# Kernel optimization log

Measured on AMD Instinct MI355X. Metric: run time of the kernel, lower is better.

## Reference

```python
import jax, jax.numpy as jnp
import numpy as np

EMBED, ACT, DETER, STOCH, HID = 1536, 10, 2048, 64, 1024
T, B = 64, 256
LN_EPS = 1e-3


def _ln(x, s, b):
    mu = jnp.mean(x, axis=-1, keepdims=True)
    var = jnp.mean(jnp.square(x - mu), axis=-1, keepdims=True)
    return (x - mu) * jax.lax.rsqrt(var + LN_EPS) * s + b


def setup_inputs() -> dict:
    key = jax.random.key(0)
    ks = jax.random.split(key, 20)
    g = lambda k, shp, fan: jax.random.normal(k, shp, jnp.float32) * (1.0 / np.sqrt(fan))
    inp = {
        "embeds": jax.random.normal(ks[0], (T, B, EMBED), jnp.float32),
        "actions": jax.random.normal(ks[1], (T, B, ACT), jnp.float32),
        "h_t": jnp.zeros((B, DETER), jnp.float32),
        "z_t": jnp.zeros((B, STOCH), jnp.float32),
        "noise": jax.random.normal(ks[2], (T, B, STOCH), jnp.float32),
        # DeterNext
        "z_mlp_w": g(ks[3], (HID // 2, STOCH), STOCH),
        "z_mlp_b": jnp.zeros((HID // 2,), jnp.float32),
        "a_mlp_w": g(ks[4], (HID // 2, ACT), ACT),  # bias=False
        "ln_za_s": jnp.ones((HID,), jnp.float32),
        "ln_za_b": jnp.zeros((HID,), jnp.float32),
        # GRUCell (torch layout: [3*deter, in])
        "gru_wih": g(ks[5], (3 * DETER, HID), HID),
        "gru_whh": g(ks[6], (3 * DETER, DETER), DETER),
        "gru_bih": jnp.zeros((3 * DETER,), jnp.float32),
        "gru_bhh": jnp.zeros((3 * DETER,), jnp.float32),
        # PosteriorNext
        "post_h_w": g(ks[7], (HID, DETER), DETER),
        "post_h_b": jnp.zeros((HID,), jnp.float32),
        "post_e_w": g(ks[8], (HID, EMBED), EMBED),
        "post_e_b": jnp.zeros((HID,), jnp.float32),
        "ln_post_s": jnp.ones((HID,), jnp.float32),
        "ln_post_b": jnp.zeros((HID,), jnp.float32),
        "post_w": g(ks[9], (2 * STOCH, HID), HID),
        "post_b": jnp.zeros((2 * STOCH,), jnp.float32),
        # PriorNext
        "prior_h_w": g(ks[10], (HID, DETER), DETER),
        "prior_h_b": jnp.zeros((HID,), jnp.float32),
        "ln_prior_s": jnp.ones((HID,), jnp.float32),
        "ln_prior_b": jnp.zeros((HID,), jnp.float32),
        "prior_w": g(ks[11], (2 * STOCH, HID), HID),
        "prior_b": jnp.zeros((2 * STOCH,), jnp.float32),
    }
    return inp


def _rssm_forward(embeds, actions, h0, z0, noise,
                  z_mlp_w, z_mlp_b, a_mlp_w, ln_za_s, ln_za_b,
                  gru_wih, gru_whh, gru_bih, gru_bhh,
                  post_h_w, post_h_b, post_e_w, post_e_b, ln_post_s, ln_post_b,
                  post_w, post_b,
                  prior_h_w, prior_h_b, ln_prior_s, ln_prior_b, prior_w, prior_b):
    def step(carry, xs):
        h, z = carry
        e, a, n = xs
        # DeterNext: concat(z_mlp(z), a_mlp(a)) -> LN -> ELU
        x = jnp.concatenate([z @ z_mlp_w.T + z_mlp_b, a @ a_mlp_w.T], axis=-1)
        za = jax.nn.elu(_ln(x, ln_za_s, ln_za_b))
        # GRUCell
        gi = za @ gru_wih.T + gru_bih
        gh = h @ gru_whh.T + gru_bhh
        ir, iu, ic = jnp.split(gi, 3, axis=-1)
        hr, hu, hc = jnp.split(gh, 3, axis=-1)
        r = jax.nn.sigmoid(ir + hr)
        u = jax.nn.sigmoid(iu + hu)
        c = jnp.tanh(ic + r * hc)
        h1 = (1.0 - u) * c + u * h
        # PosteriorNext
        p = jax.nn.elu(_ln(h1 @ post_h_w.T + post_h_b + e @ post_e_w.T + post_e_b,
                           ln_post_s, ln_post_b))
        post = p @ post_w.T + post_b  # [B, 2*stoch]
        mean, sraw = jnp.split(post, 2, axis=-1)
        std = 2.0 * jax.nn.sigmoid(sraw) + 0.1
        z1 = mean + std * n  # rsample with externally-supplied noise
        return (h1, z1), (post, h1, z1)

    (_, _), (posts, states_h, post_z_samples) = jax.lax.scan(
        step, (h0, z0), (embeds, actions, noise))
    # batch prior over all timesteps
    pr = jax.nn.elu(_ln(states_h @ prior_h_w.T + prior_h_b, ln_prior_s, ln_prior_b))
    priors = pr @ prior_w.T + prior_b  # [T, B, 2*stoch]
    features = jnp.concatenate([states_h, post_z_samples], axis=-1)  # [T,B,deter+stoch]
    return priors, posts, post_z_samples, features


def reference(embeds, actions, h_t, z_t, noise,
              z_mlp_w, z_mlp_b, a_mlp_w, ln_za_s, ln_za_b,
              gru_wih, gru_whh, gru_bih, gru_bhh,
              post_h_w, post_h_b, post_e_w, post_e_b, ln_post_s, ln_post_b,
              post_w, post_b,
              prior_h_w, prior_h_b, ln_prior_s, ln_prior_b, prior_w, prior_b):
    return _rssm_forward(embeds, actions, h_t, z_t, noise,
                         z_mlp_w, z_mlp_b, a_mlp_w, ln_za_s, ln_za_b,
                         gru_wih, gru_whh, gru_bih, gru_bhh,
                         post_h_w, post_h_b, post_e_w, post_e_b, ln_post_s, ln_post_b,
                         post_w, post_b,
                         prior_h_w, prior_h_b, ln_prior_s, ln_prior_b, prior_w, prior_b)
```

## Files before the change

kernel.cpp:

```cpp
#include <hip/hip_runtime.h>

#define LN_EPS 1e-3f

typedef short s8v __attribute__((ext_vector_type(8)));
typedef short s4v __attribute__((ext_vector_type(4)));
typedef float f4v __attribute__((ext_vector_type(4)));
typedef unsigned short u16;

__device__ __forceinline__ u16 f2bf(float f) {
  unsigned int x = __float_as_uint(f);
  x += 0x7fffu + ((x >> 16) & 1u);
  return (u16)(x >> 16);
}
__device__ __forceinline__ float bf2f(u16 u) {
  return __uint_as_float(((unsigned int)u) << 16);
}

__global__ void k_cvt(const float* __restrict__ src, u16* __restrict__ dst, int n) {
  int i = blockIdx.x * blockDim.x + threadIdx.x;
  int stride = gridDim.x * blockDim.x;
  for (; i < n; i += stride) dst[i] = f2bf(src[i]);
}

__global__ void k_pack(const float* __restrict__ wih, const float* __restrict__ whh,
                       u16* __restrict__ wp) {
  size_t i4 = ((size_t)blockIdx.x * 256 + threadIdx.x) * 4;
  int n = (int)(i4 / 3072);
  int k = (int)(i4 % 3072);
  int g = n >> 11;
  int j = n & 2047;
  s4v v;
#pragma unroll
  for (int q = 0; q < 4; ++q) {
    int kk = k + q;
    float x = 0.f;
    if (g <= 1) {
      x = (kk < 1024) ? wih[(size_t)(g * 2048 + j) * 1024 + kk]
                      : whh[(size_t)(g * 2048 + j) * 2048 + kk - 1024];
    } else if (g == 2) {
      x = (kk < 1024) ? wih[(size_t)(4096 + j) * 1024 + kk] : 0.f;
    } else {
      x = (kk >= 1024) ? whh[(size_t)(4096 + j) * 2048 + kk - 1024] : 0.f;
    }
    v[q] = (short)f2bf(x);
  }
  *(s4v*)(wp + i4) = v;
}

__global__ void k_hinit(const float* __restrict__ h0, float* __restrict__ hf,
                        u16* __restrict__ acat) {
  int i = blockIdx.x * 256 + threadIdx.x;
  int b = i >> 11, j = i & 2047;
  float v = h0[i];
  hf[i] = v;
  acat[(size_t)b * 3072 + 1024 + j] = f2bf(v);
}

template <bool AF32, bool OUTBF16, bool GRUKR>
__global__ __launch_bounds__(512) void k_gemm8(
    const void* __restrict__ Av, int lda, const u16* __restrict__ Bw, int ldb,
    int ks0, int ke0, float* __restrict__ Cf, u16* __restrict__ Cb, int ldc,
    const float* __restrict__ bias, const u16* __restrict__ extra) {
  int bx, by, ks = ks0, ke = ke0;
  if (GRUKR) {
    int hw = blockIdx.x;
    int logical = (hw & 7) * 32 + (hw >> 3);
    bx = logical & 3;
    by = logical >> 2;
    if (by < 32) { ks = 0; ke = 48; }
    else if (by < 48) { ks = 0; ke = 16; }
    else { ks = 16; ke = 48; }
  } else {
    bx = blockIdx.x;
    by = blockIdx.y;
  }
  const int tid = threadIdx.x;
  const int m0 = bx * 64;
  const int n0 = by * 128;
  __shared__ __align__(16) u16 As[64][72];
  __shared__ __align__(16) u16 Bs[128][72];
  const int lane = tid & 63;
  const int w = tid >> 6;
  const int wr = w >> 2;
  const int wc = w & 3;
  const int lr = lane & 15;
  const int lk = lane >> 4;

  f4v acc[2][2];
#pragma unroll
  for (int m = 0; m < 2; ++m)
#pragma unroll
    for (int n = 0; n < 2; ++n) acc[m][n] = (f4v)(0.0f);

  for (int s = ks; s < ke; ++s) {
    const int k0 = s << 6;
    {
      int row = tid >> 3, k8 = (tid & 7) << 3;
      if (AF32) {
        const float* ap = (const float*)Av + (size_t)(m0 + row) * lda + k0 + k8;
        float4 f0 = *(const float4*)ap;
        float4 f1 = *(const float4*)(ap + 4);
        s8v v;
        v[0] = (short)f2bf(f0.x); v[1] = (short)f2bf(f0.y);
        v[2] = (short)f2bf(f0.z); v[3] = (short)f2bf(f0.w);
        v[4] = (short)f2bf(f1.x); v[5] = (short)f2bf(f1.y);
        v[6] = (short)f2bf(f1.z); v[7] = (short)f2bf(f1.w);
        *(s8v*)&As[row][k8] = v;
      } else {
        *(s8v*)&As[row][k8] =
            *(const s8v*)((const u16*)Av + (size_t)(m0 + row) * lda + k0 + k8);
      }
    }
#pragma unroll
    for (int it = 0; it < 2; ++it) {
      int c = tid + it * 512;
      int row = c >> 3, k8 = (c & 7) << 3;
      *(s8v*)&Bs[row][k8] = *(const s8v*)(Bw + (size_t)(n0 + row) * ldb + k0 + k8);
    }
    __syncthreads();
#pragma unroll
    for (int kk = 0; kk < 2; ++kk) {
      const int koff = kk * 32 + lk * 8;
      s8v a[2], b[2];
      a[0] = *(const s8v*)&As[wr * 32 + lr][koff];
      a[1] = *(const s8v*)&As[wr * 32 + 16 + lr][koff];
      b[0] = *(const s8v*)&Bs[wc * 32 + lr][koff];
      b[1] = *(const s8v*)&Bs[wc * 32 + 16 + lr][koff];
#pragma unroll
      for (int m = 0; m < 2; ++m)
#pragma unroll
        for (int n = 0; n < 2; ++n)
          acc[m][n] =
              __builtin_amdgcn_mfma_f32_16x16x32_bf16(a[m], b[n], acc[m][n], 0, 0, 0);
    }
    __syncthreads();
  }
#pragma unroll
  for (int m = 0; m < 2; ++m) {
#pragma unroll
    for (int n = 0; n < 2; ++n) {
#pragma unroll
      for (int r = 0; r < 4; ++r) {
        int row = m0 + wr * 32 + m * 16 + lk * 4 + r;
        int col = n0 + wc * 32 + n * 16 + lr;
        float v = acc[m][n][r];
        if (bias) v += bias[col];
        if (extra) v += bf2f(extra[(size_t)row * ldc + col]);
        if (OUTBF16)
          Cb[(size_t)row * ldc + col] = f2bf(v);
        else
          Cf[(size_t)row * ldc + col] = v;
      }
    }
  }
}

__global__ __launch_bounds__(256) void k_za(
    const float* __restrict__ zsrc, const float* __restrict__ act,
    const float* __restrict__ zw, const float* __restrict__ zb,
    const float* __restrict__ aw, const float* __restrict__ lns,
    const float* __restrict__ lnb, u16* __restrict__ acat) {
  const int b = blockIdx.x, tid = threadIdx.x;
  __shared__ float zsh[64];
  __shared__ float ash[16];
  __shared__ float red[256];
  if (tid < 64) zsh[tid] = zsrc[b * 64 + tid];
  if (tid < 10) ash[tid] = act[b * 10 + tid];
  __syncthreads();
  float x[4];
#pragma unroll
  for (int i = 0; i < 2; ++i) {
    int c = tid + i * 256;
    const float* wp = zw + c * 64;
    float a = zb[c];
#pragma unroll
    for (int k = 0; k < 64; ++k) a += zsh[k] * wp[k];
    x[i] = a;
  }
#pragma unroll
  for (int i = 2; i < 4; ++i) {
    int c2 = tid + (i - 2) * 256;
    const float* wp = aw + c2 * 10;
    float a = 0.f;
#pragma unroll
    for (int k = 0; k < 10; ++k) a += ash[k] * wp[k];
    x[i] = a;
  }
  float s = x[0] + x[1] + x[2] + x[3];
  red[tid] = s;
  __syncthreads();
  for (int o = 128; o > 0; o >>= 1) {
    if (tid < o) red[tid] += red[tid + o];
    __syncthreads();
  }
  float mu = red[0] * (1.0f / 1024.0f);
  __syncthreads();
  float q = 0.f;
#pragma unroll
  for (int i = 0; i < 4; ++i) {
    float d = x[i] - mu;
    q += d * d;
  }
  red[tid] = q;
  __syncthreads();
  for (int o = 128; o > 0; o >>= 1) {
    if (tid < o) red[tid] += red[tid + o];
    __syncthreads();
  }
  float rs = rsqrtf(red[0] * (1.0f / 1024.0f) + LN_EPS);
#pragma unroll
  for (int i = 0; i < 4; ++i) {
    int c = tid + i * 256;
    float y = (x[i] - mu) * rs * lns[c] + lnb[c];
    y = y > 0.f ? y : expm1f(y);
    acat[(size_t)b * 3072 + c] = f2bf(y);
  }
}

__global__ __launch_bounds__(256) void k_gate(
    const float* __restrict__ gout, const float* __restrict__ bih,
    const float* __restrict__ bhh, float* __restrict__ hf,
    u16* __restrict__ acat, float* __restrict__ feat, int t) {
  int idx = blockIdx.x * 256 + threadIdx.x;
  int b = idx >> 11, j = idx & 2047;
  size_t rb = (size_t)b * 8192;
  float vr = gout[rb + j] + bih[j] + bhh[j];
  float vu = gout[rb + 2048 + j] + bih[2048 + j] + bhh[2048 + j];
  float ic = gout[rb + 4096 + j] + bih[4096 + j];
  float hc = gout[rb + 6144 + j] + bhh[4096 + j];
  float r = 1.f / (1.f + expf(-vr));
  float u = 1.f / (1.f + expf(-vu));
  float c = tanhf(ic + r * hc);
  float h1 = (1.f - u) * c + u * hf[idx];
  hf[idx] = h1;
  acat[(size_t)b * 3072 + 1024 + j] = f2bf(h1);
  feat[(size_t)(t * 256 + b) * 2112 + j] = h1;
}

template <bool SRCBF16>
__global__ __launch_bounds__(256) void k_lnelu(const void* __restrict__ xsrc,
                                               const float* __restrict__ s,
                                               const float* __restrict__ bb,
                                               u16* __restrict__ out) {
  int row = blockIdx.x, tid = threadIdx.x;
  __shared__ float red[256];
  float v[4];
#pragma unroll
  for (int i = 0; i < 4; ++i) {
    size_t idx = (size_t)row * 1024 + tid + i * 256;
    v[i] = SRCBF16 ? bf2f(((const u16*)xsrc)[idx]) : ((const float*)xsrc)[idx];
  }
  float sm = v[0] + v[1] + v[2] + v[3];
  red[tid] = sm;
  __syncthreads();
  for (int o = 128; o > 0; o >>= 1) {
    if (tid < o) red[tid] += red[tid + o];
    __syncthreads();
  }
  float mu = red[0] * (1.0f / 1024.0f);
  __syncthreads();
  float q = 0.f;
#pragma unroll
  for (int i = 0; i < 4; ++i) {
    float d = v[i] - mu;
    q += d * d;
  }
  red[tid] = q;
  __syncthreads();
  for (int o = 128; o > 0; o >>= 1) {
    if (tid < o) red[tid] += red[tid + o];
    __syncthreads();
  }
  float rs = rsqrtf(red[0] * (1.0f / 1024.0f) + LN_EPS);
#pragma unroll
  for (int i = 0; i < 4; ++i) {
    int c = tid + i * 256;
    float y = (v[i] - mu) * rs * s[c] + bb[c];
    y = y > 0.f ? y : expm1f(y);
    out[(size_t)row * 1024 + c] = f2bf(y);
  }
}

__global__ __launch_bounds__(512) void k_postz(
    const u16* __restrict__ Ab, const u16* __restrict__ Bw,
    const float* __restrict__ bias, float* __restrict__ posts_t,
    const float* __restrict__ noise_t, float* __restrict__ zout,
    float* __restrict__ feat, int t) {
  const int tid = threadIdx.x;
  const int m0 = blockIdx.x * 64;
  __shared__ __align__(16) u16 As[64][72];
  __shared__ __align__(16) u16 Bs[128][72];
  __shared__ float ps[64][132];
  const int lane = tid & 63;
  const int w = tid >> 6;
  const int wr = w >> 2;
  const int wc = w & 3;
  const int lr = lane & 15;
  const int lk = lane >> 4;

  f4v acc[2][2];
#pragma unroll
  for (int m = 0; m < 2; ++m)
#pragma unroll
    for (int n = 0; n < 2; ++n) acc[m][n] = (f4v)(0.0f);

  for (int s = 0; s < 16; ++s) {
    const int k0 = s << 6;
    {
      int row = tid >> 3, k8 = (tid & 7) << 3;
      *(s8v*)&As[row][k8] =
          *(const s8v*)(Ab + (size_t)(m0 + row) * 1024 + k0 + k8);
    }
#pragma unroll
    for (int it = 0; it < 2; ++it) {
      int c = tid + it * 512;
      int row = c >> 3, k8 = (c & 7) << 3;
      *(s8v*)&Bs[row][k8] = *(const s8v*)(Bw + (size_t)row * 1024 + k0 + k8);
    }
    __syncthreads();
#pragma unroll
    for (int kk = 0; kk < 2; ++kk) {
      const int koff = kk * 32 + lk * 8;
      s8v a[2], b[2];
      a[0] = *(const s8v*)&As[wr * 32 + lr][koff];
      a[1] = *(const s8v*)&As[wr * 32 + 16 + lr][koff];
      b[0] = *(const s8v*)&Bs[wc * 32 + lr][koff];
      b[1] = *(const s8v*)&Bs[wc * 32 + 16 + lr][koff];
#pragma unroll
      for (int m = 0; m < 2; ++m)
#pragma unroll
        for (int n = 0; n < 2; ++n)
          acc[m][n] =
              __builtin_amdgcn_mfma_f32_16x16x32_bf16(a[m], b[n], acc[m][n], 0, 0, 0);
    }
    __syncthreads();
  }
#pragma unroll
  for (int m = 0; m < 2; ++m) {
#pragma unroll
    for (int n = 0; n < 2; ++n) {
#pragma unroll
      for (int r = 0; r < 4; ++r) {
        int lrow = wr * 32 + m * 16 + lk * 4 + r;
        int col = wc * 32 + n * 16 + lr;
        float v = acc[m][n][r] + bias[col];
        posts_t[(size_t)(m0 + lrow) * 128 + col] = v;
        ps[lrow][col] = v;
      }
    }
  }
  __syncthreads();
#pragma unroll
  for (int q = 0; q < 8; ++q) {
    int e = tid * 8 + q;
    int row = e >> 6, j = e & 63;
    float mean = ps[row][j];
    float sraw = ps[row][64 + j];
    float sd = 2.f / (1.f + expf(-sraw)) + 0.1f;
    float z = mean + sd * noise_t[(m0 + row) * 64 + j];
    zout[(m0 + row) * 64 + j] = z;
    feat[(size_t)(t * 256 + m0 + row) * 2112 + 2048 + j] = z;
  }
}

extern "C" void kernel_launch(void* const* d_in, const int* in_sizes, int n_in,
                              void* d_out, int out_size, void* d_ws,
                              size_t ws_size, hipStream_t stream) {
  const float* embeds = (const float*)d_in[0];
  const float* actions = (const float*)d_in[1];
  const float* h_t = (const float*)d_in[2];
  const float* z_t = (const float*)d_in[3];
  const float* noise = (const float*)d_in[4];
  const float* z_mlp_w = (const float*)d_in[5];
  const float* z_mlp_b = (const float*)d_in[6];
  const float* a_mlp_w = (const float*)d_in[7];
  const float* ln_za_s = (const float*)d_in[8];
  const float* ln_za_b = (const float*)d_in[9];
  const float* gru_wih = (const float*)d_in[10];
  const float* gru_whh = (const float*)d_in[11];
  const float* gru_bih = (const float*)d_in[12];
  const float* gru_bhh = (const float*)d_in[13];
  const float* post_h_w = (const float*)d_in[14];
  const float* post_h_b = (const float*)d_in[15];
  const float* post_e_w = (const float*)d_in[16];
  const float* post_e_b = (const float*)d_in[17];
  const float* ln_post_s = (const float*)d_in[18];
  const float* ln_post_b = (const float*)d_in[19];
  const float* post_w = (const float*)d_in[20];
  const float* post_b = (const float*)d_in[21];
  const float* prior_h_w = (const float*)d_in[22];
  const float* prior_h_b = (const float*)d_in[23];
  const float* ln_prior_s = (const float*)d_in[24];
  const float* ln_prior_b = (const float*)d_in[25];
  const float* prior_w = (const float*)d_in[26];
  const float* prior_b = (const float*)d_in[27];

  float* out = (float*)d_out;
  float* out_priors = out;
  float* out_posts = out + 2097152;
  float* out_z = out + 4194304;
  float* out_feat = out + 5242880;

  char* ws = (char*)d_ws;
  size_t off = 0;
  auto alloc = [&](size_t bytes) {
    char* p = ws + off;
    off += (bytes + 255) & ~(size_t)255;
    return p;
  };
  char* regW = alloc((size_t)8192 * 3072 * 2);
  u16* wpack = (u16*)regW;
  u16* prx_b = (u16*)regW;
  u16* posth_b = (u16*)alloc((size_t)1024 * 2048 * 2);
  u16* priorh_b = (u16*)alloc((size_t)1024 * 2048 * 2);
  u16* postw_b = (u16*)alloc((size_t)128 * 1024 * 2);
  u16* priorw_b = (u16*)alloc((size_t)128 * 1024 * 2);
  u16* poste_b = (u16*)alloc((size_t)1024 * 1536 * 2);
  u16* acat = (u16*)alloc((size_t)256 * 3072 * 2);
  float* hf = (float*)alloc((size_t)256 * 2048 * 4);
  float* xbuf = (float*)alloc((size_t)256 * 1024 * 4);
  u16* p_b = (u16*)alloc((size_t)256 * 1024 * 2);
  char* regU = alloc((size_t)42 * 1024 * 1024);
  u16* e_part = (u16*)regU;
  float* gout = (float*)(regU + 33554432);
  u16* p_pr = (u16*)regU;

  k_pack<<<24576, 256, 0, stream>>>(gru_wih, gru_whh, wpack);
  k_cvt<<<512, 256, 0, stream>>>(post_h_w, posth_b, 1024 * 2048);
  k_cvt<<<512, 256, 0, stream>>>(prior_h_w, priorh_b, 1024 * 2048);
  k_cvt<<<64, 256, 0, stream>>>(post_w, postw_b, 128 * 1024);
  k_cvt<<<64, 256, 0, stream>>>(prior_w, priorw_b, 128 * 1024);
  k_cvt<<<512, 256, 0, stream>>>(post_e_w, poste_b, 1024 * 1536);
  k_hinit<<<2048, 256, 0, stream>>>(h_t, hf, acat);

  k_gemm8<true, true, false><<<dim3(256, 8), 512, 0, stream>>>(
      embeds, 1536, poste_b, 1536, 0, 24, nullptr, e_part, 1024, post_e_b,
      nullptr);

  for (int t = 0; t < 64; ++t) {
    const float* zsrc = (t == 0) ? z_t : (out_z + (size_t)(t - 1) * 16384);
    k_za<<<256, 256, 0, stream>>>(zsrc, actions + (size_t)t * 2560, z_mlp_w,
                                  z_mlp_b, a_mlp_w, ln_za_s, ln_za_b, acat);
    k_gemm8<false, false, true><<<256, 512, 0, stream>>>(
        acat, 3072, wpack, 3072, 0, 48, gout, nullptr, 8192, nullptr, nullptr);
    k_gate<<<2048, 256, 0, stream>>>(gout, gru_bih, gru_bhh, hf, acat,
                                     out_feat, t);
    k_gemm8<false, false, false><<<dim3(4, 8), 512, 0, stream>>>(
        acat + 1024, 3072, posth_b, 2048, 0, 32, xbuf, nullptr, 1024, post_h_b,
        e_part + (size_t)t * 262144);
    k_lnelu<false><<<256, 256, 0, stream>>>(xbuf, ln_post_s, ln_post_b, p_b);
    k_postz<<<4, 512, 0, stream>>>(p_b, postw_b, post_b,
                                   out_posts + (size_t)t * 32768,
                                   noise + (size_t)t * 16384,
                                   out_z + (size_t)t * 16384, out_feat, t);
  }

  k_gemm8<true, true, false><<<dim3(256, 8), 512, 0, stream>>>(
      out_feat, 2112, priorh_b, 2048, 0, 32, nullptr, prx_b, 1024, prior_h_b,
      nullptr);
  k_lnelu<true><<<16384, 256, 0, stream>>>(prx_b, ln_prior_s, ln_prior_b, p_pr);
  k_gemm8<false, false, false><<<dim3(256, 1), 512, 0, stream>>>(
      p_pr, 1024, priorw_b, 1024, 0, 16, out_priors, nullptr, 128, prior_b,
      nullptr);
}
```

Before: 8.537 ms.

## Fuse GRU gates into pre-packed GEMM, add async LDS loads, fuse posterior LN

```diff
diff --git a/kernel.cpp b/kernel.cpp
--- a/kernel.cpp
+++ b/kernel.cpp
@@ -3,7 +3,6 @@
 #define LN_EPS 1e-3f
 
 typedef short s8v __attribute__((ext_vector_type(8)));
-typedef short s4v __attribute__((ext_vector_type(4)));
 typedef float f4v __attribute__((ext_vector_type(4)));
 typedef unsigned short u16;
 
@@ -16,35 +15,69 @@
   return __uint_as_float(((unsigned int)u) << 16);
 }
 
+__device__ __forceinline__ void glds16(const u16* g, void* l) {
+  __builtin_amdgcn_global_load_lds(
+      (const __attribute__((address_space(1))) void*)g,
+      (__attribute__((address_space(3))) void*)l, 16, 0, 0);
+}
+
 __global__ void k_cvt(const float* __restrict__ src, u16* __restrict__ dst, int n) {
   int i = blockIdx.x * blockDim.x + threadIdx.x;
   int stride = gridDim.x * blockDim.x;
   for (; i < n; i += stride) dst[i] = f2bf(src[i]);
 }
 
-__global__ void k_pack(const float* __restrict__ wih, const float* __restrict__ whh,
-                       u16* __restrict__ wp) {
-  size_t i4 = ((size_t)blockIdx.x * 256 + threadIdx.x) * 4;
-  int n = (int)(i4 / 3072);
-  int k = (int)(i4 % 3072);
-  int g = n >> 11;
-  int j = n & 2047;
-  s4v v;
-#pragma unroll
-  for (int q = 0; q < 4; ++q) {
-    int kk = k + q;
-    float x = 0.f;
-    if (g <= 1) {
-      x = (kk < 1024) ? wih[(size_t)(g * 2048 + j) * 1024 + kk]
-                      : whh[(size_t)(g * 2048 + j) * 2048 + kk - 1024];
-    } else if (g == 2) {
-      x = (kk < 1024) ? wih[(size_t)(4096 + j) * 1024 + kk] : 0.f;
+__global__ void k_packgru(const float* __restrict__ wih,
+                          const float* __restrict__ whh, u16* __restrict__ wt) {
+  int u = blockIdx.x * 256 + threadIdx.x;
+  int nt = u / 73728;
+  int r1 = u % 73728;
+  int s = r1 / 1536;
+  int r2 = r1 % 1536;
+  int sub = r2 / 512;
+  int r3 = r2 % 512;
+  int ch = r3 / 64;
+  int row = r3 % 64;
+  int j = nt * 64 + row;
+  int kbase = s * 64 + ch * 8;
+  s8v v;
+#pragma unroll
+  for (int e = 0; e < 8; ++e) {
+    int kk = kbase + e;
+    float x;
+    if (sub == 0) {
+      x = kk < 1024 ? wih[(size_t)j * 1024 + kk] : whh[(size_t)j * 2048 + kk - 1024];
+    } else if (sub == 1) {
+      int jj = 2048 + j;
+      x = kk < 1024 ? wih[(size_t)jj * 1024 + kk] : whh[(size_t)jj * 2048 + kk - 1024];
     } else {
-      x = (kk >= 1024) ? whh[(size_t)(4096 + j) * 2048 + kk - 1024] : 0.f;
-    }
-    v[q] = (short)f2bf(x);
-  }
-  *(s4v*)(wp + i4) = v;
+      int jj = 4096 + j;
+      x = (s < 16) ? wih[(size_t)jj * 1024 + kk] : whh[(size_t)jj * 2048 + kk - 1024];
+    }
+    v[e] = (short)f2bf(x);
+  }
+  *(s8v*)(wt + (size_t)u * 8) = v;
+}
+
+__global__ void k_packB(const float* __restrict__ src, u16* __restrict__ dst,
+                        int K, int BN, int total) {
+  int u = blockIdx.x * 256 + threadIdx.x;
+  if (u >= total) return;
+  int ns = K >> 6;
+  int perNt = ns * 8 * BN;
+  int nt = u / perNt;
+  int r1 = u % perNt;
+  int s = r1 / (8 * BN);
+  int r2 = r1 % (8 * BN);
+  int ch = r2 / BN;
+  int row = r2 % BN;
+  int j = nt * BN + row;
+  int k = s * 64 + ch * 8;
+  const float* sp = src + (size_t)j * K + k;
+  s8v v;
+#pragma unroll
+  for (int e = 0; e < 8; ++e) v[e] = (short)f2bf(sp[e]);
+  *(s8v*)(dst + (size_t)u * 8) = v;
 }
 
 __global__ void k_hinit(const float* __restrict__ h0, float* __restrict__ hf,
@@ -56,24 +89,348 @@
   acat[(size_t)b * 3072 + 1024 + j] = f2bf(v);
 }
 
-template <bool AF32, bool OUTBF16, bool GRUKR>
+__global__ __launch_bounds__(256) void k_za(
+    const float* __restrict__ zsrc, const float* __restrict__ act,
+    const float* __restrict__ zw, const float* __restrict__ zb,
+    const float* __restrict__ aw, const float* __restrict__ lns,
+    const float* __restrict__ lnb, u16* __restrict__ acat) {
+  const int b = blockIdx.x, tid = threadIdx.x;
+  __shared__ float zsh[64];
+  __shared__ float ash[12];
+  __shared__ float wred[8];
+  if (tid < 64) zsh[tid] = zsrc[b * 64 + tid];
+  if (tid < 10) ash[tid] = act[b * 10 + tid];
+  __syncthreads();
+  float x[4];
+#pragma unroll
+  for (int i = 0; i < 2; ++i) {
+    int c = tid + i * 256;
+    const float4* wp = (const float4*)(zw + c * 64);
+    float a = zb[c];
+#pragma unroll
+    for (int k = 0; k < 16; ++k) {
+      float4 v = wp[k];
+      a += zsh[k * 4] * v.x + zsh[k * 4 + 1] * v.y + zsh[k * 4 + 2] * v.z +
+           zsh[k * 4 + 3] * v.w;
+    }
+    x[i] = a;
+  }
+#pragma unroll
+  for (int i = 2; i < 4; ++i) {
+    int c2 = tid + (i - 2) * 256;
+    const float* wp = aw + c2 * 10;
+    float a = 0.f;
+#pragma unroll
+    for (int k = 0; k < 10; ++k) a += ash[k] * wp[k];
+    x[i] = a;
+  }
+  float s = x[0] + x[1] + x[2] + x[3];
+#pragma unroll
+  for (int o = 1; o < 64; o <<= 1) s += __shfl_xor(s, o);
+  if ((tid & 63) == 0) wred[tid >> 6] = s;
+  __syncthreads();
+  float mu = (wred[0] + wred[1] + wred[2] + wred[3]) * (1.f / 1024.f);
+  float q = 0.f;
+#pragma unroll
+  for (int i = 0; i < 4; ++i) {
+    float d = x[i] - mu;
+    q += d * d;
+  }
+#pragma unroll
+  for (int o = 1; o < 64; o <<= 1) q += __shfl_xor(q, o);
+  if ((tid & 63) == 0) wred[4 + (tid >> 6)] = q;
+  __syncthreads();
+  float rs = rsqrtf((wred[4] + wred[5] + wred[6] + wred[7]) * (1.f / 1024.f) + LN_EPS);
+  int cols[4] = {tid, tid + 256, 512 + tid, 768 + tid};
+#pragma unroll
+  for (int i = 0; i < 4; ++i) {
+    int c = cols[i];
+    float y = (x[i] - mu) * rs * lns[c] + lnb[c];
+    y = y > 0.f ? y : expm1f(y);
+    acat[(size_t)b * 3072 + c] = f2bf(y);
+  }
+}
+
+__global__ __launch_bounds__(256) void k_gru(
+    const u16* __restrict__ acat_r, const u16* __restrict__ wt,
+    const float* __restrict__ bih, const float* __restrict__ bhh,
+    const float* __restrict__ hf_r, float* __restrict__ hf_w,
+    u16* __restrict__ acat_w, float* __restrict__ feat, int t) {
+  const int hw = blockIdx.x;
+  const int logical = (hw & 7) * 32 + (hw >> 3);
+  const int mg = logical & 7;
+  const int nt = logical >> 3;
+  const int m0 = mg * 32;
+  const int tid = threadIdx.x;
+  const int lane = tid & 63;
+  const int w = tid >> 6;
+  const int lr = lane & 15, lk = lane >> 4;
+
+  __shared__ __align__(16) char smem[2][28672];
+
+  const int arow = 8 * w + (lane >> 3);
+  const int acol8 = ((lane & 7) ^ (arow & 7)) * 8;
+  const u16* aSrc = acat_r + (size_t)(m0 + arow) * 3072 + acol8;
+  const u16* wtNt = wt + (size_t)nt * 48 * 3 * 4096;
+
+  f4v accr[2], accu[2], acci[2], acch[2];
+  accr[0] = accr[1] = accu[0] = accu[1] = (f4v)(0.f);
+  acci[0] = acci[1] = acch[0] = acch[1] = (f4v)(0.f);
+
+#define K1_STAGE(BB, S) { \
+    char* base = &smem[BB][0]; \
+    glds16(aSrc + (S) * 64, base + w * 1024); \
+    const u16* bsrc = wtNt + (size_t)(S) * 3 * 4096; \
+    _Pragma("unroll") for (int i = 0; i < 6; ++i) { \
+      int cf = w + i * 4; \
+      glds16(bsrc + (cf * 64 + lane) * 8, base + 4096 + cf * 1024); \
+    } }
+
+#define K1_COMP(BB, ACCX) { \
+    char* base = &smem[BB][0]; \
+    _Pragma("unroll") for (int kk = 0; kk < 2; ++kk) { \
+      int ch = kk * 4 + lk; \
+      int r0 = lr, r1 = 16 + lr; \
+      s8v a0 = *(const s8v*)(base + r0 * 128 + ((ch ^ (r0 & 7)) * 16)); \
+      s8v a1 = *(const s8v*)(base + r1 * 128 + ((ch ^ (r1 & 7)) * 16)); \
+      int rb = (w * 16 + lr) * 16; \
+      s8v br = *(const s8v*)(base + 4096 + ch * 1024 + rb); \
+      s8v bu = *(const s8v*)(base + 12288 + ch * 1024 + rb); \
+      s8v bx = *(const s8v*)(base + 20480 + ch * 1024 + rb); \
+      accr[0] = __builtin_amdgcn_mfma_f32_16x16x32_bf16(a0, br, accr[0], 0, 0, 0); \
+      accr[1] = __builtin_amdgcn_mfma_f32_16x16x32_bf16(a1, br, accr[1], 0, 0, 0); \
+      accu[0] = __builtin_amdgcn_mfma_f32_16x16x32_bf16(a0, bu, accu[0], 0, 0, 0); \
+      accu[1] = __builtin_amdgcn_mfma_f32_16x16x32_bf16(a1, bu, accu[1], 0, 0, 0); \
+      ACCX[0] = __builtin_amdgcn_mfma_f32_16x16x32_bf16(a0, bx, ACCX[0], 0, 0, 0); \
+      ACCX[1] = __builtin_amdgcn_mfma_f32_16x16x32_bf16(a1, bx, ACCX[1], 0, 0, 0); \
+    } }
+
+  K1_STAGE(0, 0)
+  int buf = 0;
+  for (int s = 0; s < 16; ++s) {
+    asm volatile("s_waitcnt vmcnt(0)" ::: "memory");
+    __builtin_amdgcn_s_barrier();
+    __builtin_amdgcn_sched_barrier(0);
+    K1_STAGE(buf ^ 1, s + 1)
+    K1_COMP(buf, acci)
+    buf ^= 1;
+  }
+  for (int s = 16; s < 48; ++s) {
+    asm volatile("s_waitcnt vmcnt(0)" ::: "memory");
+    __builtin_amdgcn_s_barrier();
+    __builtin_amdgcn_sched_barrier(0);
+    if (s + 1 < 48) K1_STAGE(buf ^ 1, s + 1)
+    K1_COMP(buf, acch)
+    buf ^= 1;
+  }
+
+  const int j = nt * 64 + w * 16 + lr;
+  const float b_ri = bih[j], b_rh = bhh[j];
+  const float b_ui = bih[2048 + j], b_uh = bhh[2048 + j];
+  const float b_ci = bih[4096 + j], b_ch = bhh[4096 + j];
+#pragma unroll
+  for (int m = 0; m < 2; ++m) {
+#pragma unroll
+    for (int r = 0; r < 4; ++r) {
+      int grow = m0 + m * 16 + lk * 4 + r;
+      float vr = accr[m][r] + b_ri + b_rh;
+      float vu = accu[m][r] + b_ui + b_uh;
+      float ic = acci[m][r] + b_ci;
+      float hc = acch[m][r] + b_ch;
+      float rg = 1.f / (1.f + expf(-vr));
+      float ug = 1.f / (1.f + expf(-vu));
+      float c = tanhf(ic + rg * hc);
+      float hold = hf_r[(size_t)grow * 2048 + j];
+      float h1 = (1.f - ug) * c + ug * hold;
+      hf_w[(size_t)grow * 2048 + j] = h1;
+      acat_w[(size_t)grow * 3072 + 1024 + j] = f2bf(h1);
+      feat[(size_t)(t * 256 + grow) * 2112 + j] = h1;
+    }
+  }
+#undef K1_STAGE
+#undef K1_COMP
+}
+
+__global__ __launch_bounds__(256) void k_post(
+    const u16* __restrict__ acat_h, const u16* __restrict__ wp,
+    const float* __restrict__ bias, const u16* __restrict__ epart_t,
+    float* __restrict__ xbuf) {
+  const int bx = blockIdx.x;
+  const int mg = bx & 7, nt = bx >> 3;
+  const int m0 = mg * 32;
+  const int tid = threadIdx.x;
+  const int lane = tid & 63;
+  const int w = tid >> 6;
+  const int lr = lane & 15, lk = lane >> 4;
+
+  __shared__ __align__(16) char smem[2][12288];
+
+  const int arow = 8 * w + (lane >> 3);
+  const int acol8 = ((lane & 7) ^ (arow & 7)) * 8;
+  const u16* aSrc = acat_h + (size_t)(m0 + arow) * 3072 + 1024 + acol8;
+  const u16* wpNt = wp + (size_t)nt * 32 * 4096;
+
+  f4v acc[2];
+  acc[0] = (f4v)(0.f);
+  acc[1] = (f4v)(0.f);
+
+#define K2_STAGE(BB, S) { \
+    char* base = &smem[BB][0]; \
+    glds16(aSrc + (S) * 64, base + w * 1024); \
+    const u16* bsrc = wpNt + (size_t)(S) * 4096; \
+    _Pragma("unroll") for (int i = 0; i < 2; ++i) { \
+      int cf = w + i * 4; \
+      glds16(bsrc + (cf * 64 + lane) * 8, base + 4096 + cf * 1024); \
+    } }
+
+  K2_STAGE(0, 0)
+  int buf = 0;
+  for (int s = 0; s < 32; ++s) {
+    asm volatile("s_waitcnt vmcnt(0)" ::: "memory");
+    __builtin_amdgcn_s_barrier();
+    __builtin_amdgcn_sched_barrier(0);
+    if (s + 1 < 32) K2_STAGE(buf ^ 1, s + 1)
+    char* base = &smem[buf][0];
+#pragma unroll
+    for (int kk = 0; kk < 2; ++kk) {
+      int ch = kk * 4 + lk;
+      int r0 = lr, r1 = 16 + lr;
+      s8v a0 = *(const s8v*)(base + r0 * 128 + ((ch ^ (r0 & 7)) * 16));
+      s8v a1 = *(const s8v*)(base + r1 * 128 + ((ch ^ (r1 & 7)) * 16));
+      s8v b = *(const s8v*)(base + 4096 + ch * 1024 + (w * 16 + lr) * 16);
+      acc[0] = __builtin_amdgcn_mfma_f32_16x16x32_bf16(a0, b, acc[0], 0, 0, 0);
+      acc[1] = __builtin_amdgcn_mfma_f32_16x16x32_bf16(a1, b, acc[1], 0, 0, 0);
+    }
+    buf ^= 1;
+  }
+  const int col = nt * 64 + w * 16 + lr;
+#pragma unroll
+  for (int m = 0; m < 2; ++m) {
+#pragma unroll
+    for (int r = 0; r < 4; ++r) {
+      int grow = m0 + m * 16 + lk * 4 + r;
+      float v = acc[m][r] + bias[col] + bf2f(epart_t[(size_t)grow * 1024 + col]);
+      xbuf[(size_t)grow * 1024 + col] = v;
+    }
+  }
+#undef K2_STAGE
+}
+
+__global__ __launch_bounds__(512) void k_postz(
+    const float* __restrict__ xb, const u16* __restrict__ pw,
+    const float* __restrict__ lns, const float* __restrict__ lnb,
+    const float* __restrict__ pb, float* __restrict__ posts_t,
+    const float* __restrict__ noise_t, float* __restrict__ zout,
+    float* __restrict__ feat, int t) {
+  const int m0 = blockIdx.x * 32;
+  const int tid = threadIdx.x;
+  const int lane = tid & 63;
+  const int w = tid >> 6;
+  const int lr = lane & 15, lk = lane >> 4;
+  __shared__ __align__(16) u16 As[2][32][64];
+  __shared__ __align__(16) u16 Bs[2][8][128][8];
+  __shared__ float lmu[32], lrs[32];
+  __shared__ float ps[32][132];
+  {
+    int row = tid >> 4, sg = tid & 15;
+    const float4* xp = (const float4*)(xb + (size_t)(m0 + row) * 1024 + sg * 64);
+    float s = 0.f, q = 0.f;
+#pragma unroll
+    for (int i = 0; i < 16; ++i) {
+      float4 v = xp[i];
+      s += v.x + v.y + v.z + v.w;
+      q += v.x * v.x + v.y * v.y + v.z * v.z + v.w * v.w;
+    }
+#pragma unroll
+    for (int o = 1; o < 16; o <<= 1) {
+      s += __shfl_xor(s, o);
+      q += __shfl_xor(q, o);
+    }
+    if (sg == 0) {
+      float mu = s * (1.f / 1024.f);
+      lmu[row] = mu;
+      lrs[row] = rsqrtf(q * (1.f / 1024.f) - mu * mu + LN_EPS);
+    }
+  }
+  __syncthreads();
+
+#define K3_STAGEA(BB, S) if (tid < 256) { \
+    int row = tid >> 3, k8 = tid & 7; \
+    const float* xp = xb + (size_t)(m0 + row) * 1024 + (S) * 64 + k8 * 8; \
+    float mu = lmu[row], rs = lrs[row]; \
+    s8v v; \
+    _Pragma("unroll") for (int e = 0; e < 8; ++e) { \
+      int c = (S) * 64 + k8 * 8 + e; \
+      float y = (xp[e] - mu) * rs * lns[c] + lnb[c]; \
+      y = y > 0.f ? y : expm1f(y); \
+      v[e] = (short)f2bf(y); \
+    } \
+    *(s8v*)((char*)&As[BB][0][0] + row * 128 + ((k8 ^ (row & 7)) * 16)) = v; }
+
+#define K3_STAGEB(BB, S) { \
+    const u16* bsrc = pw + (size_t)(S) * 8192; \
+    glds16(bsrc + (((w >> 1) * 128 + (w & 1) * 64 + lane) * 8), \
+           (char*)&Bs[BB][0][0][0] + w * 1024); \
+    glds16(bsrc + ((((w >> 1) + 4) * 128 + (w & 1) * 64 + lane) * 8), \
+           (char*)&Bs[BB][0][0][0] + w * 1024 + 8192); }
+
+  f4v acc[2];
+  acc[0] = (f4v)(0.f);
+  acc[1] = (f4v)(0.f);
+  K3_STAGEA(0, 0)
+  K3_STAGEB(0, 0)
+  __syncthreads();
+  int buf = 0;
+  for (int s = 0; s < 16; ++s) {
+    if (s + 1 < 16) {
+      K3_STAGEA(buf ^ 1, s + 1)
+      K3_STAGEB(buf ^ 1, s + 1)
+    }
+#pragma unroll
+    for (int kk = 0; kk < 2; ++kk) {
+      int ch = kk * 4 + lk;
+      int r0 = lr, r1 = 16 + lr;
+      s8v a0 = *(const s8v*)((char*)&As[buf][0][0] + r0 * 128 + ((ch ^ (r0 & 7)) * 16));
+      s8v a1 = *(const s8v*)((char*)&As[buf][0][0] + r1 * 128 + ((ch ^ (r1 & 7)) * 16));
+      s8v b = *(const s8v*)((char*)&Bs[buf][0][0][0] + ch * 2048 + (w * 16 + lr) * 16);
+      acc[0] = __builtin_amdgcn_mfma_f32_16x16x32_bf16(a0, b, acc[0], 0, 0, 0);
+      acc[1] = __builtin_amdgcn_mfma_f32_16x16x32_bf16(a1, b, acc[1], 0, 0, 0);
+    }
+    __syncthreads();
+    buf ^= 1;
+  }
+#pragma unroll
+  for (int m = 0; m < 2; ++m) {
+#pragma unroll
+    for (int r = 0; r < 4; ++r) {
+      int row = m * 16 + lk * 4 + r;
+      int col = w * 16 + lr;
+      float v = acc[m][r] + pb[col];
+      posts_t[(size_t)(m0 + row) * 128 + col] = v;
+      ps[row][col] = v;
+    }
+  }
+  __syncthreads();
+#pragma unroll
+  for (int q = 0; q < 4; ++q) {
+    int e = q * 512 + tid;
+    int row = e >> 6, j = e & 63;
+    float mean = ps[row][j], sraw = ps[row][64 + j];
+    float sd = 2.f / (1.f + expf(-sraw)) + 0.1f;
+    float z = mean + sd * noise_t[(m0 + row) * 64 + j];
+    zout[(m0 + row) * 64 + j] = z;
+    feat[(size_t)(t * 256 + m0 + row) * 2112 + 2048 + j] = z;
+  }
+#undef K3_STAGEA
+#undef K3_STAGEB
+}
+
+template <bool AF32, bool OUTBF16>
 __global__ __launch_bounds__(512) void k_gemm8(
     const void* __restrict__ Av, int lda, const u16* __restrict__ Bw, int ldb,
-    int ks0, int ke0, float* __restrict__ Cf, u16* __restrict__ Cb, int ldc,
-    const float* __restrict__ bias, const u16* __restrict__ extra) {
-  int bx, by, ks = ks0, ke = ke0;
-  if (GRUKR) {
-    int hw = blockIdx.x;
-    int logical = (hw & 7) * 32 + (hw >> 3);
-    bx = logical & 3;
-    by = logical >> 2;
-    if (by < 32) { ks = 0; ke = 48; }
-    else if (by < 48) { ks = 0; ke = 16; }
-    else { ks = 16; ke = 48; }
-  } else {
-    bx = blockIdx.x;
-    by = blockIdx.y;
-  }
+    int nstage, float* __restrict__ Cf, u16* __restrict__ Cb, int ldc,
+    const float* __restrict__ bias) {
+  const int bx = blockIdx.x, by = blockIdx.y;
   const int tid = threadIdx.x;
   const int m0 = bx * 64;
   const int n0 = by * 128;
@@ -92,7 +449,7 @@
 #pragma unroll
     for (int n = 0; n < 2; ++n) acc[m][n] = (f4v)(0.0f);
 
-  for (int s = ks; s < ke; ++s) {
+  for (int s = 0; s < nstage; ++s) {
     const int k0 = s << 6;
     {
       int row = tid >> 3, k8 = (tid & 7) << 3;
@@ -145,7 +502,6 @@
         int col = n0 + wc * 32 + n * 16 + lr;
         float v = acc[m][n][r];
         if (bias) v += bias[col];
-        if (extra) v += bf2f(extra[(size_t)row * ldc + col]);
         if (OUTBF16)
           Cb[(size_t)row * ldc + col] = f2bf(v);
         else
@@ -155,90 +511,7 @@
   }
 }
 
-__global__ __launch_bounds__(256) void k_za(
-    const float* __restrict__ zsrc, const float* __restrict__ act,
-    const float* __restrict__ zw, const float* __restrict__ zb,
-    const float* __restrict__ aw, const float* __restrict__ lns,
-    const float* __restrict__ lnb, u16* __restrict__ acat) {
-  const int b = blockIdx.x, tid = threadIdx.x;
-  __shared__ float zsh[64];
-  __shared__ float ash[16];
-  __shared__ float red[256];
-  if (tid < 64) zsh[tid] = zsrc[b * 64 + tid];
-  if (tid < 10) ash[tid] = act[b * 10 + tid];
-  __syncthreads();
-  float x[4];
-#pragma unroll
-  for (int i = 0; i < 2; ++i) {
-    int c = tid + i * 256;
-    const float* wp = zw + c * 64;
-    float a = zb[c];
-#pragma unroll
-    for (int k = 0; k < 64; ++k) a += zsh[k] * wp[k];
-    x[i] = a;
-  }
-#pragma unroll
-  for (int i = 2; i < 4; ++i) {
-    int c2 = tid + (i - 2) * 256;
-    const float* wp = aw + c2 * 10;
-    float a = 0.f;
-#pragma unroll
-    for (int k = 0; k < 10; ++k) a += ash[k] * wp[k];
-    x[i] = a;
-  }
-  float s = x[0] + x[1] + x[2] + x[3];
-  red[tid] = s;
-  __syncthreads();
-  for (int o = 128; o > 0; o >>= 1) {
-    if (tid < o) red[tid] += red[tid + o];
-    __syncthreads();
-  }
-  float mu = red[0] * (1.0f / 1024.0f);
-  __syncthreads();
-  float q = 0.f;
-#pragma unroll
-  for (int i = 0; i < 4; ++i) {
-    float d = x[i] - mu;
-    q += d * d;
-  }
-  red[tid] = q;
-  __syncthreads();
-  for (int o = 128; o > 0; o >>= 1) {
-    if (tid < o) red[tid] += red[tid + o];
-    __syncthreads();
-  }
-  float rs = rsqrtf(red[0] * (1.0f / 1024.0f) + LN_EPS);
-#pragma unroll
-  for (int i = 0; i < 4; ++i) {
-    int c = tid + i * 256;
-    float y = (x[i] - mu) * rs * lns[c] + lnb[c];
-    y = y > 0.f ? y : expm1f(y);
-    acat[(size_t)b * 3072 + c] = f2bf(y);
-  }
-}
-
-__global__ __launch_bounds__(256) void k_gate(
-    const float* __restrict__ gout, const float* __restrict__ bih,
-    const float* __restrict__ bhh, float* __restrict__ hf,
-    u16* __restrict__ acat, float* __restrict__ feat, int t) {
-  int idx = blockIdx.x * 256 + threadIdx.x;
-  int b = idx >> 11, j = idx & 2047;
-  size_t rb = (size_t)b * 8192;
-  float vr = gout[rb + j] + bih[j] + bhh[j];
-  float vu = gout[rb + 2048 + j] + bih[2048 + j] + bhh[2048 + j];
-  float ic = gout[rb + 4096 + j] + bih[4096 + j];
-  float hc = gout[rb + 6144 + j] + bhh[4096 + j];
-  float r = 1.f / (1.f + expf(-vr));
-  float u = 1.f / (1.f + expf(-vu));
-  float c = tanhf(ic + r * hc);
-  float h1 = (1.f - u) * c + u * hf[idx];
-  hf[idx] = h1;
-  acat[(size_t)b * 3072 + 1024 + j] = f2bf(h1);
-  feat[(size_t)(t * 256 + b) * 2112 + j] = h1;
-}
-
-template <bool SRCBF16>
-__global__ __launch_bounds__(256) void k_lnelu(const void* __restrict__ xsrc,
+__global__ __launch_bounds__(256) void k_lnelu(const u16* __restrict__ xsrc,
                                                const float* __restrict__ s,
                                                const float* __restrict__ bb,
                                                u16* __restrict__ out) {
@@ -248,7 +521,7 @@
 #pragma unroll
   for (int i = 0; i < 4; ++i) {
     size_t idx = (size_t)row * 1024 + tid + i * 256;
-    v[i] = SRCBF16 ? bf2f(((const u16*)xsrc)[idx]) : ((const float*)xsrc)[idx];
+    v[i] = bf2f(xsrc[idx]);
   }
   float sm = v[0] + v[1] + v[2] + v[3];
   red[tid] = sm;
@@ -278,88 +551,6 @@
     float y = (v[i] - mu) * rs * s[c] + bb[c];
     y = y > 0.f ? y : expm1f(y);
     out[(size_t)row * 1024 + c] = f2bf(y);
-  }
-}
-
-__global__ __launch_bounds__(512) void k_postz(
-    const u16* __restrict__ Ab, const u16* __restrict__ Bw,
-    const float* __restrict__ bias, float* __restrict__ posts_t,
-    const float* __restrict__ noise_t, float* __restrict__ zout,
-    float* __restrict__ feat, int t) {
-  const int tid = threadIdx.x;
-  const int m0 = blockIdx.x * 64;
-  __shared__ __align__(16) u16 As[64][72];
-  __shared__ __align__(16) u16 Bs[128][72];
-  __shared__ float ps[64][132];
-  const int lane = tid & 63;
-  const int w = tid >> 6;
-  const int wr = w >> 2;
-  const int wc = w & 3;
-  const int lr = lane & 15;
-  const int lk = lane >> 4;
-
-  f4v acc[2][2];
-#pragma unroll
-  for (int m = 0; m < 2; ++m)
-#pragma unroll
-    for (int n = 0; n < 2; ++n) acc[m][n] = (f4v)(0.0f);
-
-  for (int s = 0; s < 16; ++s) {
-    const int k0 = s << 6;
-    {
-      int row = tid >> 3, k8 = (tid & 7) << 3;
-      *(s8v*)&As[row][k8] =
-          *(const s8v*)(Ab + (size_t)(m0 + row) * 1024 + k0 + k8);
-    }
-#pragma unroll
-    for (int it = 0; it < 2; ++it) {
-      int c = tid + it * 512;
-      int row = c >> 3, k8 = (c & 7) << 3;
-      *(s8v*)&Bs[row][k8] = *(const s8v*)(Bw + (size_t)row * 1024 + k0 + k8);
-    }
-    __syncthreads();
-#pragma unroll
-    for (int kk = 0; kk < 2; ++kk) {
-      const int koff = kk * 32 + lk * 8;
-      s8v a[2], b[2];
-      a[0] = *(const s8v*)&As[wr * 32 + lr][koff];
-      a[1] = *(const s8v*)&As[wr * 32 + 16 + lr][koff];
-      b[0] = *(const s8v*)&Bs[wc * 32 + lr][koff];
-      b[1] = *(const s8v*)&Bs[wc * 32 + 16 + lr][koff];
-#pragma unroll
-      for (int m = 0; m < 2; ++m)
-#pragma unroll
-        for (int n = 0; n < 2; ++n)
-          acc[m][n] =
-              __builtin_amdgcn_mfma_f32_16x16x32_bf16(a[m], b[n], acc[m][n], 0, 0, 0);
-    }
-    __syncthreads();
-  }
-#pragma unroll
-  for (int m = 0; m < 2; ++m) {
-#pragma unroll
-    for (int n = 0; n < 2; ++n) {
-#pragma unroll
-      for (int r = 0; r < 4; ++r) {
-        int lrow = wr * 32 + m * 16 + lk * 4 + r;
-        int col = wc * 32 + n * 16 + lr;
-        float v = acc[m][n][r] + bias[col];
-        posts_t[(size_t)(m0 + lrow) * 128 + col] = v;
-        ps[lrow][col] = v;
-      }
-    }
-  }
-  __syncthreads();
-#pragma unroll
-  for (int q = 0; q < 8; ++q) {
-    int e = tid * 8 + q;
-    int row = e >> 6, j = e & 63;
-    float mean = ps[row][j];
-    float sraw = ps[row][64 + j];
-    float sd = 2.f / (1.f + expf(-sraw)) + 0.1f;
-    float z = mean + sd * noise_t[(m0 + row) * 64 + j];
-    zout[(m0 + row) * 64 + j] = z;
-    feat[(size_t)(t * 256 + m0 + row) * 2112 + 2048 + j] = z;
   }
 }
 
@@ -408,58 +599,55 @@
     off += (bytes + 255) & ~(size_t)255;
     return p;
   };
-  char* regW = alloc((size_t)8192 * 3072 * 2);
-  u16* wpack = (u16*)regW;
+  char* regW = alloc((size_t)32 * 48 * 3 * 4096 * 2);
+  u16* wt = (u16*)regW;
   u16* prx_b = (u16*)regW;
-  u16* posth_b = (u16*)alloc((size_t)1024 * 2048 * 2);
+  u16* posthP = (u16*)alloc((size_t)1024 * 2048 * 2);
+  u16* postwP = (u16*)alloc((size_t)128 * 1024 * 2);
+  u16* poste_b = (u16*)alloc((size_t)1024 * 1536 * 2);
   u16* priorh_b = (u16*)alloc((size_t)1024 * 2048 * 2);
-  u16* postw_b = (u16*)alloc((size_t)128 * 1024 * 2);
   u16* priorw_b = (u16*)alloc((size_t)128 * 1024 * 2);
-  u16* poste_b = (u16*)alloc((size_t)1024 * 1536 * 2);
-  u16* acat = (u16*)alloc((size_t)256 * 3072 * 2);
-  float* hf = (float*)alloc((size_t)256 * 2048 * 4);
+  u16* acat0 = (u16*)alloc((size_t)256 * 3072 * 2);
+  u16* acat1 = (u16*)alloc((size_t)256 * 3072 * 2);
+  float* hf0 = (float*)alloc((size_t)256 * 2048 * 4);
+  float* hf1 = (float*)alloc((size_t)256 * 2048 * 4);
   float* xbuf = (float*)alloc((size_t)256 * 1024 * 4);
-  u16* p_b = (u16*)alloc((size_t)256 * 1024 * 2);
-  char* regU = alloc((size_t)42 * 1024 * 1024);
+  char* regU = alloc((size_t)16384 * 1024 * 2);
   u16* e_part = (u16*)regU;
-  float* gout = (float*)(regU + 33554432);
   u16* p_pr = (u16*)regU;
 
-  k_pack<<<24576, 256, 0, stream>>>(gru_wih, gru_whh, wpack);
-  k_cvt<<<512, 256, 0, stream>>>(post_h_w, posth_b, 1024 * 2048);
+  u16* acat[2] = {acat0, acat1};
+  float* hf[2] = {hf0, hf1};
+
+  k_packgru<<<9216, 256, 0, stream>>>(gru_wih, gru_whh, wt);
+  k_packB<<<1024, 256, 0, stream>>>(post_h_w, posthP, 2048, 64, 262144);
+  k_packB<<<64, 256, 0, stream>>>(post_w, postwP, 1024, 128, 16384);
+  k_cvt<<<512, 256, 0, stream>>>(post_e_w, poste_b, 1024 * 1536);
   k_cvt<<<512, 256, 0, stream>>>(prior_h_w, priorh_b, 1024 * 2048);
-  k_cvt<<<64, 256, 0, stream>>>(post_w, postw_b, 128 * 1024);
   k_cvt<<<64, 256, 0, stream>>>(prior_w, priorw_b, 128 * 1024);
-  k_cvt<<<512, 256, 0, stream>>>(post_e_w, poste_b, 1024 * 1536);
-  k_hinit<<<2048, 256, 0, stream>>>(h_t, hf, acat);
-
-  k_gemm8<true, true, false><<<dim3(256, 8), 512, 0, stream>>>(
-      embeds, 1536, poste_b, 1536, 0, 24, nullptr, e_part, 1024, post_e_b,
-      nullptr);
+  k_hinit<<<2048, 256, 0, stream>>>(h_t, hf0, acat0);
+
+  k_gemm8<true, true><<<dim3(256, 8), 512, 0, stream>>>(
+      embeds, 1536, poste_b, 1536, 24, nullptr, e_part, 1024, post_e_b);
 
   for (int t = 0; t < 64; ++t) {
+    const int rI = t & 1, wI = rI ^ 1;
     const float* zsrc = (t == 0) ? z_t : (out_z + (size_t)(t - 1) * 16384);
     k_za<<<256, 256, 0, stream>>>(zsrc, actions + (size_t)t * 2560, z_mlp_w,
-                                  z_mlp_b, a_mlp_w, ln_za_s, ln_za_b, acat);
-    k_gemm8<false, false, true><<<256, 512, 0, stream>>>(
-        acat, 3072, wpack, 3072, 0, 48, gout, nullptr, 8192, nullptr, nullptr);
-    k_gate<<<2048, 256, 0, stream>>>(gout, gru_bih, gru_bhh, hf, acat,
-                                     out_feat, t);
-    k_gemm8<false, false, false><<<dim3(4, 8), 512, 0, stream>>>(
-        acat + 1024, 3072, posth_b, 2048, 0, 32, xbuf, nullptr, 1024, post_h_b,
-        e_part + (size_t)t * 262144);
-    k_lnelu<false><<<256, 256, 0, stream>>>(xbuf, ln_post_s, ln_post_b, p_b);
-    k_postz<<<4, 512, 0, stream>>>(p_b, postw_b, post_b,
+                                  z_mlp_b, a_mlp_w, ln_za_s, ln_za_b, acat[rI]);
+    k_gru<<<256, 256, 0, stream>>>(acat[rI], wt, gru_bih, gru_bhh, hf[rI],
+                                   hf[wI], acat[wI], out_feat, t);
+    k_post<<<128, 256, 0, stream>>>(acat[wI], posthP, post_h_b,
+                                    e_part + (size_t)t * 262144, xbuf);
+    k_postz<<<8, 512, 0, stream>>>(xbuf, postwP, ln_post_s, ln_post_b, post_b,
                                    out_posts + (size_t)t * 32768,
                                    noise + (size_t)t * 16384,
                                    out_z + (size_t)t * 16384, out_feat, t);
   }
 
-  k_gemm8<true, true, false><<<dim3(256, 8), 512, 0, stream>>>(
-      out_feat, 2112, priorh_b, 2048, 0, 32, nullptr, prx_b, 1024, prior_h_b,
-      nullptr);
-  k_lnelu<true><<<16384, 256, 0, stream>>>(prx_b, ln_prior_s, ln_prior_b, p_pr);
-  k_gemm8<false, false, false><<<dim3(256, 1), 512, 0, stream>>>(
-      p_pr, 1024, priorw_b, 1024, 0, 16, out_priors, nullptr, 128, prior_b,
-      nullptr);
-}
+  k_gemm8<true, true><<<dim3(256, 8), 512, 0, stream>>>(
+      out_feat, 2112, priorh_b, 2048, 32, nullptr, prx_b, 1024, prior_h_b);
+  k_lnelu<<<16384, 256, 0, stream>>>(prx_b, ln_prior_s, ln_prior_b, p_pr);
+  k_gemm8<false, false><<<dim3(256, 1), 512, 0, stream>>>(
+      p_pr, 1024, priorw_b, 1024, 16, out_priors, nullptr, 128, prior_b);
+}
```

Measured after the change: 7.119 ms. -16.6%, faster.
